# Kernel optimization log

Measured on AMD Instinct MI355X. Metric: run time of the kernel, lower is better.

## Reference

```python
import jax, jax.numpy as jnp
import numpy as np

N, E = 50000, 800000
IN, HID, HEADS, LAT = 128, 64, 4, 32
NEG_SLOPE = 0.2  # PyG GATv2Conv default negative_slope


def _glorot(key, shape):
    fan_in, fan_out = shape[0], shape[-1]
    lim = (6.0 / (fan_in + fan_out)) ** 0.5
    return jax.random.uniform(key, shape, jnp.float32, -lim, lim)


def setup_inputs() -> dict:
    keys = jax.random.split(jax.random.key(0), 10)
    x = jax.random.normal(keys[0], (N, IN), jnp.float32)
    edge_index = jax.random.randint(keys[1], (2, E), 0, N, jnp.int32)
    return {
        "x": x,
        "edge_index": edge_index,
        # layer 1: in -> hidden, heads=HEADS, concat=True
        "W_l1": _glorot(keys[2], (IN, HEADS * HID)),
        "W_r1": _glorot(keys[3], (IN, HEADS * HID)),
        "att1": _glorot(keys[4], (HEADS, HID)),
        "bias1": jnp.zeros((HEADS * HID,), jnp.float32),
        # layer 2: heads*hidden -> latent, heads=1, concat=False
        "W_l2": _glorot(keys[5], (HEADS * HID, LAT)),
        "W_r2": _glorot(keys[6], (HEADS * HID, LAT)),
        "att2": _glorot(keys[7], (1, LAT)),
        "bias2": jnp.zeros((LAT,), jnp.float32),
    }


def gatv2_layer(x, src, dst, W_l, W_r, att, bias, heads, out_ch, concat):
    """PyG GATv2Conv (eval mode, add_self_loops already applied to src/dst)."""
    n = x.shape[0]
    xl = (x @ W_l).reshape(n, heads, out_ch)  # source transform (messages)
    xr = (x @ W_r).reshape(n, heads, out_ch)  # target transform
    # per-edge attention logits: a^T LeakyReLU(xl[j] + xr[i])
    e = jax.nn.leaky_relu(xl[src] + xr[dst], NEG_SLOPE)  # [E, H, C]
    score = jnp.einsum('ehc,hc->eh', e, att)             # [E, H]
    # segment softmax over incoming edges of each dst node
    smax = jax.ops.segment_max(score, dst, num_segments=n)   # [N, H]
    ex = jnp.exp(score - smax[dst])
    denom = jax.ops.segment_sum(ex, dst, num_segments=n)     # [N, H]
    alpha = ex / denom[dst]                                  # [E, H]
    # scatter-add weighted source features
    out = jax.ops.segment_sum(xl[src] * alpha[..., None], dst, num_segments=n)
    out = out.reshape(n, heads * out_ch) if concat else out.mean(axis=1)
    return out + bias


def reference(x, edge_index, W_l1, W_r1, att1, bias1, W_l2, W_r2, att2, bias2):
    n = x.shape[0]
    # GATv2Conv adds self loops by default
    loops = jnp.arange(n, dtype=edge_index.dtype)
    src = jnp.concatenate([edge_index[0], loops])
    dst = jnp.concatenate([edge_index[1], loops])
    h = jax.nn.elu(gatv2_layer(x, src, dst, W_l1, W_r1, att1, bias1, HEADS, HID, True))
    z = gatv2_layer(h, src, dst, W_l2, W_r2, att2, bias2, 1, LAT, False)
    # decode: sigmoid(<z[row], z[col]>) over the original edges
    row, col = edge_index[0], edge_index[1]
    pred = jax.nn.sigmoid(jnp.sum(z[row] * z[col], axis=1))
    return pred
```

## Files before the change

### kernel.cpp

```cpp
#include <hip/hip_runtime.h>
#include <hip/hip_fp16.h>
#include <math.h>

#define N_NODES 50000
#define N_EDGES 800000
#define EP (N_EDGES + N_NODES)
#define IN_CH 128
#define HID 64
#define HEADS 4
#define F1 (HEADS * HID)
#define LAT 32
#define NEG 0.2f
#define CAP 64
#define NW (512 * 128 + 64 * 256)
#define ZQ 12500
#define G1B ((N_NODES + 31) / 32)
#define SCB ((EP + 255) / 256)
#define TB (G1B + SCB)

typedef __attribute__((ext_vector_type(8))) short short8;
typedef __attribute__((ext_vector_type(8))) unsigned short ushort8v;
typedef __attribute__((ext_vector_type(4))) float f32x4;
typedef __attribute__((ext_vector_type(2))) float f32x2;
typedef __attribute__((ext_vector_type(4))) unsigned int uint4v;

__device__ __forceinline__ unsigned short f2bf(float f) {
    unsigned int x = __float_as_uint(f);
    x += 0x7fffu + ((x >> 16) & 1u);
    return (unsigned short)(x >> 16);
}
__device__ __forceinline__ float bf2f(unsigned short u) {
    return __uint_as_float(((unsigned int)u) << 16);
}
__device__ __forceinline__ float h2f(unsigned short u) {
    return __half2float(__ushort_as_half(u));
}
__device__ __forceinline__ f32x2 up2(unsigned w) {
    f32x2 r;
    r[0] = __uint_as_float(w << 16);
    r[1] = __uint_as_float(w & 0xffff0000u);
    return r;
}
__device__ __forceinline__ f32x4 mfma_bf16(short8 a, short8 b, f32x4 c) {
    return __builtin_amdgcn_mfma_f32_16x16x32_bf16(a, b, c, 0, 0, 0);
}
__device__ __forceinline__ unsigned cvt_pk_bf16(float lo, float hi) {
    unsigned r;
    asm("v_cvt_pk_bf16_f32 %0, %1, %2" : "=v"(r) : "v"(lo), "v"(hi));
    return r;
}
__device__ __forceinline__ short8 pack_bf16x8(float4 A, float4 B) {
    uint4v u;
    u[0] = cvt_pk_bf16(A.x, A.y);
    u[1] = cvt_pk_bf16(A.z, A.w);
    u[2] = cvt_pk_bf16(B.x, B.y);
    u[3] = cvt_pk_bf16(B.z, B.w);
    return __builtin_bit_cast(short8, u);
}

__global__ void conv_w_zero(const float* __restrict__ Wl1, const float* __restrict__ Wr1,
                            const float* __restrict__ Wl2, const float* __restrict__ Wr2,
                            unsigned short* __restrict__ Wt1, unsigned short* __restrict__ Wt2,
                            int4* __restrict__ zbase) {
    int idx = blockIdx.x * 256 + threadIdx.x;
    if (idx < ZQ) zbase[idx] = make_int4(0, 0, 0, 0);
    if (idx < 512 * 128) {
        int n = idx >> 7, k = idx & 127;
        float v = (n < 256) ? Wl1[(size_t)k * 256 + n] : Wr1[(size_t)k * 256 + (n - 256)];
        Wt1[idx] = f2bf(v);
    } else if (idx < NW) {
        int j = idx - 512 * 128;
        int n = j >> 8, k = j & 255;
        float v = (n < 32) ? Wl2[(size_t)k * 32 + n] : Wr2[(size_t)k * 32 + (n - 32)];
        Wt2[j] = f2bf(v);
    }
}

__global__ __launch_bounds__(256) void gemm1_scatter(const float* __restrict__ x,
                                                     const unsigned short* __restrict__ Wt1,
                                                     unsigned short* __restrict__ xlh,
                                                     unsigned short* __restrict__ xrh,
                                                     const int* __restrict__ ei,
                                                     int* __restrict__ cnt,
                                                     unsigned short* __restrict__ srcsP) {
    int bid = blockIdx.x;
    bool isScatter;
    int wid;
    if (bid < 3 * G1B) {
        isScatter = (bid % 3 != 1);
        wid = isScatter ? (bid - (bid + 1) / 3) : (bid / 3);
    } else {
        isScatter = true;
        wid = bid - G1B;
    }

    if (isScatter) {
        long e = (long)wid * 256 + threadIdx.x;
        if (e >= EP) return;
        int s, d;
        if (e < N_EDGES) { s = ei[e]; d = ei[N_EDGES + e]; }
        else             { s = d = (int)(e - N_EDGES); }
        int pos = atomicAdd(&cnt[d], 1);
        if (pos < CAP)
            __builtin_nontemporal_store((unsigned short)s, &srcsP[(d << 6) + pos]);
        return;
    }

    int wave = threadIdx.x >> 6;
    int lane = threadIdx.x & 63;
    int quad = lane >> 4, lo = lane & 15;
    int row0 = wid * 32;
    int colw = wave * 128;
    int rB0 = min(row0 + lo, N_NODES - 1);
    int rB1 = min(row0 + 16 + lo, N_NODES - 1);
    f32x4 acc[2][8];
#pragma unroll
    for (int rt = 0; rt < 2; rt++)
#pragma unroll
        for (int ct = 0; ct < 8; ct++) acc[rt][ct] = (f32x4){0.f, 0.f, 0.f, 0.f};
#pragma unroll
    for (int ks = 0; ks < 4; ks++) {
        int koff = ks * 32 + quad * 8;
        float4 fa0 = *(const float4*)(x + (size_t)rB0 * IN_CH + koff);
        float4 fb0 = *(const float4*)(x + (size_t)rB0 * IN_CH + koff + 4);
        float4 fa1 = *(const float4*)(x + (size_t)rB1 * IN_CH + koff);
        float4 fb1 = *(const float4*)(x + (size_t)rB1 * IN_CH + koff + 4);
        short8 b0 = pack_bf16x8(fa0, fb0);
        short8 b1 = pack_bf16x8(fa1, fb1);
#pragma unroll
        for (int ct = 0; ct < 8; ct++) {
            short8 a = *(const short8*)(Wt1 + (size_t)(colw + ct * 16 + lo) * IN_CH + koff);
            acc[0][ct] = mfma_bf16(a, b0, acc[0][ct]);
            acc[1][ct] = mfma_bf16(a, b1, acc[1][ct]);
        }
    }
#pragma unroll
    for (int rt = 0; rt < 2; rt++) {
        int node = row0 + rt * 16 + lo;
        if (node < N_NODES) {
#pragma unroll
            for (int ct = 0; ct < 8; ct++) {
                int feat = colw + ct * 16 + quad * 4;
                uint2 u;
                u.x = cvt_pk_bf16(acc[rt][ct][0], acc[rt][ct][1]);
                u.y = cvt_pk_bf16(acc[rt][ct][2], acc[rt][ct][3]);
                if (feat < F1)
                    *(uint2*)(xlh + (size_t)node * F1 + feat) = u;
                else
                    *(uint2*)(xrh + (size_t)node * F1 + (feat - F1)) = u;
            }
        }
    }
}

__global__ __launch_bounds__(256) void fused_l1(const unsigned short* __restrict__ xlh,
                                                const unsigned short* __restrict__ xrh,
                                                unsigned short* __restrict__ hbf,
                                                const unsigned short* __restrict__ srcsP,
                                                const int* __restrict__ cnt,
                                                const float* __restrict__ att,
                                                const float* __restrict__ bias) {
    int wave = threadIdx.x >> 6;
    int lane = threadIdx.x & 63;
    int h = lane >> 5;
    int c = lane & 31;
    int c0 = c << 3;
    int d = blockIdx.x * 4 + wave;
    if (d >= N_NODES) return;
    uint4v xru = *(const uint4v*)(xrh + (size_t)d * F1 + c0);
    float4 atA = *(const float4*)(att + c0);
    float4 atB = *(const float4*)(att + c0 + 4);
    f32x2 xr2v[4], at2[4];
#pragma unroll
    for (int p = 0; p < 4; p++) xr2v[p] = up2(xru[p]);
    at2[0] = (f32x2){atA.x, atA.y};
    at2[1] = (f32x2){atA.z, atA.w};
    at2[2] = (f32x2){atB.x, atB.y};
    at2[3] = (f32x2){atB.z, atB.w};
    const f32x2 negv = (f32x2){NEG, NEG};
    int start = d << 6;
    int dg    = min(CAP, __builtin_amdgcn_readfirstlane(cnt[d]));
    float l = 0.f;
    f32x2 acc2[4] = {};
    int jj = h;
    int s = srcsP[start + jj];
    uint4v raw = *(const uint4v*)(xlh + (size_t)s * F1 + c0);
    int sN = srcsP[start + jj + 2];
    int iters = (dg + 1) >> 1;
    for (int k = 0; k < iters; k++) {
        uint4v cr = raw;
        raw = *(const uint4v*)(xlh + (size_t)sN * F1 + c0);
        sN = srcsP[start + jj + 4];
        f32x2 ap[4];
        f32x2 sp = (f32x2){0.f, 0.f};
#pragma unroll
        for (int p = 0; p < 4; p++) {
            ap[p] = up2(cr[p]);
            f32x2 v = ap[p] + xr2v[p];
            f32x2 lk = __builtin_elementwise_max(v, v * negv);
            sp = lk * at2[p] + sp;
        }
        float sc = sp[0] + sp[1];
        sc += __shfl_xor(sc, 1);
        sc += __shfl_xor(sc, 2);
        sc += __shfl_xor(sc, 4);
        float ex = (jj < dg) ? __expf(sc) : 0.f;
        l += ex;
        f32x2 ex2 = (f32x2){ex, ex};
#pragma unroll
        for (int p = 0; p < 4; p++) acc2[p] = ex2 * ap[p] + acc2[p];
        jj += 2;
    }
    float acc[8];
#pragma unroll
    for (int p = 0; p < 4; p++) { acc[2 * p] = acc2[p][0]; acc[2 * p + 1] = acc2[p][1]; }
    l += __shfl_xor(l, 32);
#pragma unroll
    for (int i = 0; i < 8; i++) acc[i] += __shfl_xor(acc[i], 32);
    if (h == 0) {
        float inv = 1.0f / l;
        float4 bA = *(const float4*)(bias + c0);
        float4 bB = *(const float4*)(bias + c0 + 4);
        float b8[8] = {bA.x, bA.y, bA.z, bA.w, bB.x, bB.y, bB.z, bB.w};
        ushort8v ho;
#pragma unroll
        for (int i = 0; i < 8; i++) {
            float o = acc[i] * inv + b8[i];
            o = o > 0.f ? o : __expf(o) - 1.0f;
            ho[i] = (unsigned short)f2bf(o);
        }
        *(ushort8v*)(hbf + (size_t)d * F1 + c0) = ho;
    }
}

__global__ __launch_bounds__(256) void gemm2_mfma(const unsigned short* __restrict__ hbf,
                                                  const unsigned short* __restrict__ Wt2,
                                                  __half* __restrict__ xl2h,
                                                  float* __restrict__ xr2) {
    int wave = threadIdx.x >> 6;
    int lane = threadIdx.x & 63;
    int quad = lane >> 4, lo = lane & 15;
    int row0 = blockIdx.x * 64 + wave * 16;
    int rB = min(row0 + lo, N_NODES - 1);
    f32x4 acc[4];
#pragma unroll
    for (int ct = 0; ct < 4; ct++) acc[ct] = (f32x4){0.f, 0.f, 0.f, 0.f};
#pragma unroll
    for (int ks = 0; ks < 8; ks++) {
        int koff = ks * 32 + quad * 8;
        short8 b = *(const short8*)(hbf + (size_t)rB * F1 + koff);
#pragma unroll
        for (int ct = 0; ct < 4; ct++) {
            short8 a = *(const short8*)(Wt2 + (size_t)(ct * 16 + lo) * F1 + koff);
            acc[ct] = mfma_bf16(a, b, acc[ct]);
        }
    }
    int node = row0 + lo;
    if (node < N_NODES) {
#pragma unroll
        for (int ct = 0; ct < 4; ct++) {
            int feat = ct * 16 + quad * 4;
            if (feat < LAT) {
                ushort4 u;
                u.x = __half_as_ushort(__float2half_rn(acc[ct][0]));
                u.y = __half_as_ushort(__float2half_rn(acc[ct][1]));
                u.z = __half_as_ushort(__float2half_rn(acc[ct][2]));
                u.w = __half_as_ushort(__float2half_rn(acc[ct][3]));
                *(ushort4*)((unsigned short*)xl2h + (size_t)node * LAT + feat) = u;
            } else {
                float4 f = make_float4(acc[ct][0], acc[ct][1], acc[ct][2], acc[ct][3]);
                *(float4*)(xr2 + (size_t)node * LAT + (feat - LAT)) = f;
            }
        }
    }
}

__global__ __launch_bounds__(256) void fused_l2(const __half* __restrict__ xl2h,
                                                const float* __restrict__ xr2,
                                                const unsigned short* __restrict__ srcsP,
                                                const int* __restrict__ cnt,
                                                const float* __restrict__ att,
                                                const float* __restrict__ bias,
                                                __half* __restrict__ zh) {
    int wave = threadIdx.x >> 6;
    int lane = threadIdx.x & 63;
    int q = lane >> 4;
    int c = lane & 15;
    int c2 = c << 1;
    int d = blockIdx.x * 4 + wave;
    if (d >= N_NODES) return;
    float xr0 = xr2[(size_t)d * LAT + c2];
    float xr1v = xr2[(size_t)d * LAT + c2 + 1];
    float av0 = att[c2], av1 = att[c2 + 1];
    float a60 = 0.6f * av0, a40 = 0.4f * av0;
    float a61 = 0.6f * av1, a41 = 0.4f * av1;
    int start = d << 6;
    int dg    = min(CAP, __builtin_amdgcn_readfirstlane(cnt[d]));
    float l = 0.f, acc0 = 0.f, acc1 = 0.f;
    int jj = q;
    int s = srcsP[start + jj];
    __half2 raw = *(const __half2*)(xl2h + (size_t)s * LAT + c2);
    int sN = srcsP[start + jj + 4];
    int iters = (dg + 3) >> 2;
    for (int k = 0; k < iters; k++) {
        __half2 cr = raw;
        raw = *(const __half2*)(xl2h + (size_t)sN * LAT + c2);
        sN = srcsP[start + jj + 8];
        float a0 = __half2float(cr.x), a1 = __half2float(cr.y);
        float v0 = a0 + xr0;
        float v1 = a1 + xr1v;
        float sc = 0.f;
        sc = fmaf(v0, a60, sc);
        sc = fmaf(fabsf(v0), a40, sc);
        sc = fmaf(v1, a61, sc);
        sc = fmaf(fabsf(v1), a41, sc);
        sc += __shfl_xor(sc, 1);
        sc += __shfl_xor(sc, 2);
        sc += __shfl_xor(sc, 4);
        sc += __shfl_xor(sc, 8);
        float ex = (jj < dg) ? __expf(sc) : 0.f;
        l += ex;
        acc0 = fmaf(ex, a0, acc0);
        acc1 = fmaf(ex, a1, acc1);
        jj += 4;
    }
    l += __shfl_xor(l, 16); acc0 += __shfl_xor(acc0, 16); acc1 += __shfl_xor(acc1, 16);
    l += __shfl_xor(l, 32); acc0 += __shfl_xor(acc0, 32); acc1 += __shfl_xor(acc1, 32);
    if (q == 0) {
        __half2 o;
        o.x = __float2half_rn(acc0 / l + bias[c2]);
        o.y = __float2half_rn(acc1 / l + bias[c2 + 1]);
        *(__half2*)(zh + (size_t)d * LAT + c2) = o;
    }
}

__global__ __launch_bounds__(256) void decode(const __half* __restrict__ zh,
                                              const int* __restrict__ ei,
                                              float* __restrict__ out) {
    int g = threadIdx.x >> 2;
    int lane = threadIdx.x & 3;
    long e = (long)blockIdx.x * 64 + g;
    if (e >= N_EDGES) return;
    int r = ei[e], c = ei[N_EDGES + e];
    int cc = lane << 3;
    ushort8v ur = *(const ushort8v*)((const unsigned short*)zh + (size_t)r * LAT + cc);
    ushort8v uc = *(const ushort8v*)((const unsigned short*)zh + (size_t)c * LAT + cc);
    float v = 0.f;
#pragma unroll
    for (int i = 0; i < 8; i++) {
        v += h2f(ur[i]) * h2f(uc[i]);
    }
    v += __shfl_xor(v, 1);
    v += __shfl_xor(v, 2);
    if (lane == 0) out[e] = 1.0f / (1.0f + __expf(-v));
}

extern "C" void kernel_launch(void* const* d_in, const int* in_sizes, int n_in,
                              void* d_out, int out_size, void* d_ws, size_t ws_size,
                              hipStream_t stream) {
    const float* x    = (const float*)d_in[0];
    const int*   ei   = (const int*)d_in[1];
    const float* Wl1  = (const float*)d_in[2];
    const float* Wr1  = (const float*)d_in[3];
    const float* att1 = (const float*)d_in[4];
    const float* b1   = (const float*)d_in[5];
    const float* Wl2  = (const float*)d_in[6];
    const float* Wr2  = (const float*)d_in[7];
    const float* att2 = (const float*)d_in[8];
    const float* b2   = (const float*)d_in[9];
    float* out = (float*)d_out;

    unsigned short* xrh = (unsigned short*)d_ws;
    unsigned short* hbf = xrh + (size_t)N_NODES * F1;
    unsigned short* xlh = hbf + (size_t)N_NODES * F1;
    int* cnt = (int*)(xlh + (size_t)N_NODES * F1);
    unsigned short* srcsP = (unsigned short*)(cnt + N_NODES);
    unsigned short* Wt1 = srcsP + (size_t)N_NODES * CAP + 16;
    unsigned short* Wt2 = Wt1 + 512 * 128;
    __half* xl2h = (__half*)xlh;
    float*  xr2  = (float*)(xl2h + (size_t)N_NODES * LAT);
    __half* zh   = (__half*)(xr2 + (size_t)N_NODES * LAT);

    conv_w_zero<<<(NW + 255) / 256, 256, 0, stream>>>(Wl1, Wr1, Wl2, Wr2, Wt1, Wt2,
                                                      (int4*)cnt);

    gemm1_scatter<<<TB, 256, 0, stream>>>(x, Wt1, xlh, xrh, ei, cnt, srcsP);

    fused_l1<<<(N_NODES + 3) / 4, 256, 0, stream>>>(xlh, xrh, hbf, srcsP, cnt, att1, b1);

    gemm2_mfma<<<(N_NODES + 63) / 64, 256, 0, stream>>>(hbf, Wt2, xl2h, xr2);
    fused_l2<<<(N_NODES + 3) / 4, 256, 0, stream>>>(xl2h, xr2, srcsP, cnt, att2, b2, zh);

    decode<<<(N_EDGES + 63) / 64, 256, 0, stream>>>(zh, ei, out);
}
```

Before: 283.9 us.

## Replace global-atomic edge scatter with per-block LDS-counted destination range scans

The edge bucketing no longer uses one thread per edge doing global atomics on the per-node counters. Instead, 64 blocks each own a contiguous range of 782 destination nodes, scan the whole destination array, and count with LDS atomics. Each block then writes the self loops and the final counts, so the separate counter-zeroing pass is removed. Every scan block reads the full 800K destination list (64x redundant reads), and the whole scatter now runs on only 64 blocks. Those blocks may become the critical path next to the GEMM blocks.

```diff
diff --git a/kernel.cpp b/kernel.cpp
--- a/kernel.cpp
+++ b/kernel.cpp
@@ -13,10 +13,10 @@
 #define NEG 0.2f
 #define CAP 64
 #define NW (512 * 128 + 64 * 256)
-#define ZQ 12500
 #define G1B ((N_NODES + 31) / 32)
-#define SCB ((EP + 255) / 256)
-#define TB (G1B + SCB)
+#define NSCAN 64
+#define DPB 782
+#define TB (NSCAN + G1B)
 
 typedef __attribute__((ext_vector_type(8))) short short8;
 typedef __attribute__((ext_vector_type(8))) unsigned short ushort8v;
@@ -58,12 +58,10 @@
     return __builtin_bit_cast(short8, u);
 }
 
-__global__ void conv_w_zero(const float* __restrict__ Wl1, const float* __restrict__ Wr1,
-                            const float* __restrict__ Wl2, const float* __restrict__ Wr2,
-                            unsigned short* __restrict__ Wt1, unsigned short* __restrict__ Wt2,
-                            int4* __restrict__ zbase) {
+__global__ void conv_w(const float* __restrict__ Wl1, const float* __restrict__ Wr1,
+                       const float* __restrict__ Wl2, const float* __restrict__ Wr2,
+                       unsigned short* __restrict__ Wt1, unsigned short* __restrict__ Wt2) {
     int idx = blockIdx.x * 256 + threadIdx.x;
-    if (idx < ZQ) zbase[idx] = make_int4(0, 0, 0, 0);
     if (idx < 512 * 128) {
         int n = idx >> 7, k = idx & 127;
         float v = (n < 256) ? Wl1[(size_t)k * 256 + n] : Wr1[(size_t)k * 256 + (n - 256)];
@@ -76,35 +74,77 @@
     }
 }
 
-__global__ __launch_bounds__(256) void gemm1_scatter(const float* __restrict__ x,
-                                                     const unsigned short* __restrict__ Wt1,
-                                                     unsigned short* __restrict__ xlh,
-                                                     unsigned short* __restrict__ xrh,
-                                                     const int* __restrict__ ei,
-                                                     int* __restrict__ cnt,
-                                                     unsigned short* __restrict__ srcsP) {
+__global__ __launch_bounds__(256) void gemm1_scan(const float* __restrict__ x,
+                                                  const unsigned short* __restrict__ Wt1,
+                                                  unsigned short* __restrict__ xlh,
+                                                  unsigned short* __restrict__ xrh,
+                                                  const int* __restrict__ ei,
+                                                  int* __restrict__ cnt,
+                                                  unsigned short* __restrict__ srcsP) {
+    __shared__ int lcnt[DPB];
     int bid = blockIdx.x;
-    bool isScatter;
-    int wid;
-    if (bid < 3 * G1B) {
-        isScatter = (bid % 3 != 1);
-        wid = isScatter ? (bid - (bid + 1) / 3) : (bid / 3);
-    } else {
-        isScatter = true;
-        wid = bid - G1B;
-    }
-
-    if (isScatter) {
-        long e = (long)wid * 256 + threadIdx.x;
-        if (e >= EP) return;
-        int s, d;
-        if (e < N_EDGES) { s = ei[e]; d = ei[N_EDGES + e]; }
-        else             { s = d = (int)(e - N_EDGES); }
-        int pos = atomicAdd(&cnt[d], 1);
-        if (pos < CAP)
-            __builtin_nontemporal_store((unsigned short)s, &srcsP[(d << 6) + pos]);
+    if (bid < NSCAN) {
+        int d0 = bid * DPB;
+        for (int i = threadIdx.x; i < DPB; i += 256) lcnt[i] = 0;
+        __syncthreads();
+        long e = threadIdx.x;
+        for (; e + 768 < N_EDGES; e += 1024) {
+            int dv0 = ei[N_EDGES + e];
+            int dv1 = ei[N_EDGES + e + 256];
+            int dv2 = ei[N_EDGES + e + 512];
+            int dv3 = ei[N_EDGES + e + 768];
+            unsigned r0 = (unsigned)(dv0 - d0);
+            if (r0 < DPB) {
+                int pos = atomicAdd(&lcnt[r0], 1);
+                if (pos < CAP)
+                    __builtin_nontemporal_store((unsigned short)ei[e],
+                                                &srcsP[(dv0 << 6) + pos]);
+            }
+            unsigned r1 = (unsigned)(dv1 - d0);
+            if (r1 < DPB) {
+                int pos = atomicAdd(&lcnt[r1], 1);
+                if (pos < CAP)
+                    __builtin_nontemporal_store((unsigned short)ei[e + 256],
+                                                &srcsP[(dv1 << 6) + pos]);
+            }
+            unsigned r2 = (unsigned)(dv2 - d0);
+            if (r2 < DPB) {
+                int pos = atomicAdd(&lcnt[r2], 1);
+                if (pos < CAP)
+                    __builtin_nontemporal_store((unsigned short)ei[e + 512],
+                                                &srcsP[(dv2 << 6) + pos]);
+            }
+            unsigned r3 = (unsigned)(dv3 - d0);
+            if (r3 < DPB) {
+                int pos = atomicAdd(&lcnt[r3], 1);
+                if (pos < CAP)
+                    __builtin_nontemporal_store((unsigned short)ei[e + 768],
+                                                &srcsP[(dv3 << 6) + pos]);
+            }
+        }
+        for (; e < N_EDGES; e += 256) {
+            int dv = ei[N_EDGES + e];
+            unsigned r = (unsigned)(dv - d0);
+            if (r < DPB) {
+                int pos = atomicAdd(&lcnt[r], 1);
+                if (pos < CAP)
+                    __builtin_nontemporal_store((unsigned short)ei[e],
+                                                &srcsP[(dv << 6) + pos]);
+            }
+        }
+        __syncthreads();
+        for (int i = threadIdx.x; i < DPB; i += 256) {
+            int d = d0 + i;
+            if (d < N_NODES) {
+                int pos = lcnt[i];
+                if (pos < CAP)
+                    __builtin_nontemporal_store((unsigned short)d, &srcsP[(d << 6) + pos]);
+                cnt[d] = pos + 1;
+            }
+        }
         return;
     }
+    int wid = bid - NSCAN;
 
     int wave = threadIdx.x >> 6;
     int lane = threadIdx.x & 63;
@@ -381,10 +421,9 @@
     float*  xr2  = (float*)(xl2h + (size_t)N_NODES * LAT);
     __half* zh   = (__half*)(xr2 + (size_t)N_NODES * LAT);
 
-    conv_w_zero<<<(NW + 255) / 256, 256, 0, stream>>>(Wl1, Wr1, Wl2, Wr2, Wt1, Wt2,
-                                                      (int4*)cnt);
-
-    gemm1_scatter<<<TB, 256, 0, stream>>>(x, Wt1, xlh, xrh, ei, cnt, srcsP);
+    conv_w<<<(NW + 255) / 256, 256, 0, stream>>>(Wl1, Wr1, Wl2, Wr2, Wt1, Wt2);
+
+    gemm1_scan<<<TB, 256, 0, stream>>>(x, Wt1, xlh, xrh, ei, cnt, srcsP);
 
     fused_l1<<<(N_NODES + 3) / 4, 256, 0, stream>>>(xlh, xrh, hbf, srcsP, cnt, att1, b1);
 
```

New measurement: 967.5 us. +240.8%, slower.
